# Kernel optimization log

Hardware: AMD Instinct MI355X
Metric: run time of the kernel (lower is better)

## Reference

```python
import jax, jax.numpy as jnp
import numpy as np

EPS = 1e-6
N_HEAD = 16

def alibi_slopes(n_head):
    # standard ALiBi geometric slopes for power-of-2 head counts
    start = 2.0 ** (-8.0 / n_head)
    return (start ** np.arange(1, n_head + 1)).astype(np.float32)

def rsig(x):
    # rational sigmoid sigma(x) = 0.5 * (x / (|x| + 1) + 1)
    return 0.5 * (x / (jnp.abs(x) + 1.0) + 1.0)

def mr_norm(x, w):
    # RationalMR: x / (mean(|x|) + eps) * weight
    return x / (jnp.mean(jnp.abs(x), axis=-1, keepdims=True) + EPS) * w


def setup_inputs() -> dict:
    key = jax.random.key(0)
    ks = jax.random.split(key, 6)
    d_model, d_ffn = 1024, 4096
    B, T = 1, 2048
    x = jax.random.normal(ks[0], (B, T, d_model), dtype=jnp.float32)
    s = 0.02
    w_qkv = jax.random.normal(ks[1], (3 * d_model, d_model), dtype=jnp.float32) * s
    w_out = jax.random.normal(ks[2], (d_model, d_model), dtype=jnp.float32) * s
    w_merged = jax.random.normal(ks[3], (2 * d_ffn, d_model), dtype=jnp.float32) * s
    w3 = jax.random.normal(ks[4], (d_model, d_ffn), dtype=jnp.float32) * s
    norm1_w = jnp.ones((d_model,), dtype=jnp.float32)
    norm2_w = jnp.ones((d_model,), dtype=jnp.float32)
    return {"x": x, "w_qkv": w_qkv, "w_out": w_out, "w_merged": w_merged,
            "w3": w3, "norm1_w": norm1_w, "norm2_w": norm2_w}


def reference(x, w_qkv, w_out, w_merged, w3, norm1_w, norm2_w):
    B, T, C = x.shape
    H = N_HEAD
    D = C // H
    scale = 1.0 / jnp.sqrt(jnp.float32(D))

    # --- attention sub-block ---
    h = mr_norm(x, norm1_w)
    qkv = (h @ w_qkv.T).reshape(B, T, 3, H, D).transpose(2, 0, 3, 1, 4)  # [3,B,H,T,D]
    q, k, v = qkv[0], qkv[1], qkv[2]
    scores = jnp.einsum('bhtd,bhsd->bhts', q, k) * scale  # [B,H,T,T]
    pos = jnp.arange(T)
    rel = jnp.abs(pos[:, None] - pos[None, :]).astype(jnp.float32)
    slopes = jnp.asarray(alibi_slopes(H))
    scores = scores - rel[None, None] * slopes[None, :, None, None]
    causal = pos[None, :] > pos[:, None]  # mask j > i
    scores = jnp.where(causal[None, None], jnp.float32(-10000.0), scores)
    # rational softmax: sigma(s)^4 / (sum sigma(s)^4 + eps)
    p4 = rsig(scores) ** 4
    probs = p4 / (jnp.sum(p4, axis=-1, keepdims=True) + EPS)
    attn = jnp.einsum('bhts,bhsd->bhtd', probs, v)  # [B,H,T,D]
    attn = attn.transpose(0, 2, 1, 3).reshape(B, T, C)
    x = x + attn @ w_out.T

    # --- FFN sub-block (rational SwiGLU) ---
    h2 = mr_norm(x, norm2_w)
    merged = h2 @ w_merged.T
    gate, val = jnp.split(merged, 2, axis=-1)
    hidden = gate * rsig(gate) * val
    x = x + hidden @ w3.T
    return x
```

## Files before the change

kernel.cpp:

```cpp
#include <hip/hip_runtime.h>
#include <hip/hip_bf16.h>
#include <stdint.h>

typedef unsigned int u32;
typedef unsigned short u16;
typedef __attribute__((ext_vector_type(8))) short bf16x8;
typedef __attribute__((ext_vector_type(4))) float f32x4;

#define MFMA(a, b, c) __builtin_amdgcn_mfma_f32_16x16x32_bf16(a, b, c, 0, 0, 0)

__device__ __forceinline__ u16 f2bf(float f) {
  u32 u = __float_as_uint(f);
  return (u16)((u + 0x7FFFu + ((u >> 16) & 1u)) >> 16);
}
__device__ __forceinline__ float bf2f(u16 h) {
  return __uint_as_float(((u32)h) << 16);
}
__device__ __forceinline__ float rsig_fast(float sc) {
  return 0.5f + 0.5f * sc * __builtin_amdgcn_rcpf(fabsf(sc) + 1.f);
}
__device__ __forceinline__ void async16(void* lds, const void* g) {
  __builtin_amdgcn_global_load_lds((const __attribute__((address_space(1))) u32*)g,
                                   (__attribute__((address_space(3))) u32*)lds, 16, 0, 0);
}

__global__ __launch_bounds__(256) void to_bf16_all(const float* __restrict__ s0, u16* __restrict__ d0,
                                                   const float* __restrict__ s1, u16* __restrict__ d1,
                                                   const float* __restrict__ s2, u16* __restrict__ d2,
                                                   const float* __restrict__ s3, u16* __restrict__ d3) {
  int b = blockIdx.x;
  const float* src; u16* dst;
  if (b < 1536)      { src = s0; dst = d0; }
  else if (b < 2048) { src = s1; dst = d1; b -= 1536; }
  else if (b < 6144) { src = s2; dst = d2; b -= 2048; }
  else               { src = s3; dst = d3; b -= 6144; }
  const size_t i = (size_t)b * 256 + threadIdx.x;
  const float4 a = ((const float4*)src)[2 * i];
  const float4 c = ((const float4*)src)[2 * i + 1];
  ushort4 o0, o1;
  o0.x = f2bf(a.x); o0.y = f2bf(a.y); o0.z = f2bf(a.z); o0.w = f2bf(a.w);
  o1.x = f2bf(c.x); o1.y = f2bf(c.y); o1.z = f2bf(c.z); o1.w = f2bf(c.w);
  ((ushort4*)dst)[2 * i] = o0;
  ((ushort4*)dst)[2 * i + 1] = o1;
}

__global__ __launch_bounds__(256) void mrnorm(const float* __restrict__ x,
                                              const float* __restrict__ wg,
                                              u16* __restrict__ out) {
  const int row = blockIdx.x;
  const int tid = threadIdx.x;
  const float4 v = ((const float4*)(x + (size_t)row * 1024))[tid];
  float s = fabsf(v.x) + fabsf(v.y) + fabsf(v.z) + fabsf(v.w);
#pragma unroll
  for (int off = 1; off < 64; off <<= 1) s += __shfl_xor(s, off);
  __shared__ float red[4];
  if ((tid & 63) == 0) red[tid >> 6] = s;
  __syncthreads();
  const float inv = 1.f / ((red[0] + red[1] + red[2] + red[3]) * (1.f / 1024.f) + 1e-6f);
  const float4 g = ((const float4*)wg)[tid];
  ushort4 o;
  o.x = f2bf(v.x * inv * g.x);
  o.y = f2bf(v.y * inv * g.y);
  o.z = f2bf(v.z * inv * g.z);
  o.w = f2bf(v.w * inv * g.w);
  ((ushort4*)out)[(size_t)row * 256 + tid] = o;
}

template <int EPI, bool DBUF>
__global__ __launch_bounds__(256) void gemm_bt(const u16* __restrict__ A, int lda,
                                               const u16* __restrict__ B, int ldb,
                                               void* __restrict__ C,
                                               const float* __restrict__ resid,
                                               int M, int N, int K) {
  __shared__ __align__(16) u16 As[(DBUF ? 2 : 1) * 128 * 64];
  __shared__ __align__(16) u16 Bs[(DBUF ? 2 : 1) * 128 * 64];
  const int tid = threadIdx.x;
  const int lane = tid & 63;
  const int w = tid >> 6;
  const int wr = (w >> 1) << 6;
  const int wc = (w & 1) << 6;
  const int nbn = N >> 7;
  const int m0 = (blockIdx.x / nbn) << 7;
  const int n0 = (blockIdx.x % nbn) << 7;
  const int l15 = lane & 15;
  const int lhi = lane >> 4;
  A += (size_t)blockIdx.y * K;
  B += (size_t)blockIdx.y * K;

  f32x4 acc[4][4] = {};

  auto stage = [&](int buf, int k0) {
#pragma unroll
    for (int p = 0; p < 4; ++p) {
      const int c = p * 256 + tid;
      const int row = c >> 3;
      const int cb = (c & 7) << 4;
      const int src = cb ^ ((row & 7) << 4);
      async16((char*)As + buf * 16384 + c * 16,
              (const char*)A + ((size_t)(m0 + row) * lda + k0) * 2 + src);
      async16((char*)Bs + buf * 16384 + c * 16,
              (const char*)B + ((size_t)(n0 + row) * ldb + k0) * 2 + src);
    }
  };
  auto compute = [&](int buf) {
#pragma unroll
    for (int kk = 0; kk < 2; ++kk) {
      bf16x8 af[4], bfr[4];
#pragma unroll
      for (int m = 0; m < 4; ++m) {
        const int row = wr + (m << 4) + l15;
        const int off = row * 128 + (((kk << 6) + (lhi << 4)) ^ ((row & 7) << 4));
        af[m] = *(const bf16x8*)((const char*)As + buf * 16384 + off);
      }
#pragma unroll
      for (int n = 0; n < 4; ++n) {
        const int row = wc + (n << 4) + l15;
        const int off = row * 128 + (((kk << 6) + (lhi << 4)) ^ ((row & 7) << 4));
        bfr[n] = *(const bf16x8*)((const char*)Bs + buf * 16384 + off);
      }
#pragma unroll
      for (int m = 0; m < 4; ++m)
#pragma unroll
        for (int n = 0; n < 4; ++n)
          acc[m][n] = MFMA(af[m], bfr[n], acc[m][n]);
    }
  };

  if (DBUF) {
    stage(0, 0);
    __syncthreads();
    int cur = 0;
    for (int k0 = 0; k0 < K; k0 += 64) {
      if (k0 + 64 < K) stage(cur ^ 1, k0 + 64);
      compute(cur);
      __syncthreads();
      cur ^= 1;
    }
  } else {
    for (int k0 = 0; k0 < K; k0 += 64) {
      stage(0, k0);
      __syncthreads();
      compute(0);
      __syncthreads();
    }
  }

  u16* Cp = (u16*)C + (size_t)blockIdx.y * M * N;
#pragma unroll
  for (int m = 0; m < 4; ++m) {
#pragma unroll
    for (int n = 0; n < 4; ++n) {
      const int col = n0 + wc + (n << 4) + l15;
#pragma unroll
      for (int r = 0; r < 4; ++r) {
        const int row = m0 + wr + (m << 4) + (lhi << 2) + r;
        const float v = acc[m][n][r];
        if (EPI == 0) {
          Cp[(size_t)row * N + col] = f2bf(v);
        } else {
          const size_t idx = (size_t)row * N + col;
          ((float*)C)[idx] = resid[idx] + v;
        }
      }
    }
  }
}

__global__ __launch_bounds__(256) void gemm_ffn1(const u16* __restrict__ A,
                                                 const u16* __restrict__ B,
                                                 u16* __restrict__ hid) {
  __shared__ __align__(16) u16 As[2][128 * 64];
  __shared__ __align__(16) u16 Bg[2][64 * 64];
  __shared__ __align__(16) u16 Bv[2][64 * 64];
  const int tid = threadIdx.x;
  const int lane = tid & 63;
  const int w = tid >> 6;
  const int wr = (w >> 1) << 6;
  const int wc = (w & 1) << 5;
  const int m0 = (blockIdx.x >> 6) << 7;
  const int n0 = (blockIdx.x & 63) << 6;
  const int l15 = lane & 15;
  const int lhi = lane >> 4;

  f32x4 ag[4][2] = {};
  f32x4 av[4][2] = {};

  auto stage = [&](int buf, int k0) {
#pragma unroll
    for (int p = 0; p < 4; ++p) {
      const int c = p * 256 + tid;
      const int row = c >> 3;
      const int cb = (c & 7) << 4;
      const int src = cb ^ ((row & 7) << 4);
      async16((char*)As[buf] + c * 16,
              (const char*)A + ((size_t)(m0 + row) * 1024 + k0) * 2 + src);
    }
#pragma unroll
    for (int p = 0; p < 2; ++p) {
      const int c = p * 256 + tid;
      const int row = c >> 3;
      const int cb = (c & 7) << 4;
      const int src = cb ^ ((row & 7) << 4);
      async16((char*)Bg[buf] + c * 16,
              (const char*)B + ((size_t)(n0 + row) * 1024 + k0) * 2 + src);
      async16((char*)Bv[buf] + c * 16,
              (const char*)B + ((size_t)(4096 + n0 + row) * 1024 + k0) * 2 + src);
    }
  };
  auto compute = [&](int buf) {
#pragma unroll
    for (int kk = 0; kk < 2; ++kk) {
      bf16x8 af[4], bgf[2], bvf[2];
#pragma unroll
      for (int m = 0; m < 4; ++m) {
        const int row = wr + (m << 4) + l15;
        const int off = row * 128 + (((kk << 6) + (lhi << 4)) ^ ((row & 7) << 4));
        af[m] = *(const bf16x8*)((const char*)As[buf] + off);
      }
#pragma unroll
      for (int n = 0; n < 2; ++n) {
        const int row = wc + (n << 4) + l15;
        const int off = row * 128 + (((kk << 6) + (lhi << 4)) ^ ((row & 7) << 4));
        bgf[n] = *(const bf16x8*)((const char*)Bg[buf] + off);
        bvf[n] = *(const bf16x8*)((const char*)Bv[buf] + off);
      }
#pragma unroll
      for (int m = 0; m < 4; ++m)
#pragma unroll
        for (int n = 0; n < 2; ++n) {
          ag[m][n] = MFMA(af[m], bgf[n], ag[m][n]);
          av[m][n] = MFMA(af[m], bvf[n], av[m][n]);
        }
    }
  };

  stage(0, 0);
  __syncthreads();
  int cur = 0;
  for (int k0 = 0; k0 < 1024; k0 += 64) {
    if (k0 + 64 < 1024) stage(cur ^ 1, k0 + 64);
    compute(cur);
    __syncthreads();
    cur ^= 1;
  }

#pragma unroll
  for (int m = 0; m < 4; ++m) {
#pragma unroll
    for (int n = 0; n < 2; ++n) {
      const int col = n0 + wc + (n << 4) + l15;
#pragma unroll
      for (int r = 0; r < 4; ++r) {
        const int row = m0 + wr + (m << 4) + (lhi << 2) + r;
        const float g = ag[m][n][r];
        const float v = av[m][n][r];
        hid[(size_t)row * 4096 + col] = f2bf(g * rsig_fast(g) * v);
      }
    }
  }
}

template <int NC, bool BF16OUT>
__global__ __launch_bounds__(256) void splitk_reduce(const u16* __restrict__ part,
                                                     size_t cstride,
                                                     const float* __restrict__ resid,
                                                     void* __restrict__ out) {
  const size_t i = ((size_t)blockIdx.x * 256 + threadIdx.x) * 8;
  float acc[8];
  if constexpr (BF16OUT) {
#pragma unroll
    for (int j = 0; j < 8; ++j) acc[j] = 0.f;
  } else {
    const float4 r0 = *(const float4*)(resid + i);
    const float4 r1 = *(const float4*)(resid + i + 4);
    acc[0] = r0.x; acc[1] = r0.y; acc[2] = r0.z; acc[3] = r0.w;
    acc[4] = r1.x; acc[5] = r1.y; acc[6] = r1.z; acc[7] = r1.w;
  }
#pragma unroll
  for (int c = 0; c < NC; ++c) {
    const uint4 p = *(const uint4*)(part + (size_t)c * cstride + i);
    const u16* ps = (const u16*)&p;
#pragma unroll
    for (int j = 0; j < 8; ++j) acc[j] += bf2f(ps[j]);
  }
  if constexpr (BF16OUT) {
    u16 ob[8];
#pragma unroll
    for (int j = 0; j < 8; ++j) ob[j] = f2bf(acc[j]);
    *(uint4*)((u16*)out + i) = *(const uint4*)ob;
  } else {
    float4 o0 = {acc[0], acc[1], acc[2], acc[3]};
    float4 o1 = {acc[4], acc[5], acc[6], acc[7]};
    *(float4*)((float*)out + i) = o0;
    *(float4*)((float*)out + i + 4) = o1;
  }
}

__global__ __launch_bounds__(256) void transpose_v(const u16* __restrict__ qkv,
                                                   u16* __restrict__ vt) {
  __shared__ __align__(16) u16 tile[64][72];
  const int head = blockIdx.x >> 5;
  const int t0 = (blockIdx.x & 31) << 6;
  const int tid = threadIdx.x;
  const int row = tid >> 2;
  const int cb = (tid & 3) << 4;
  const u16* src = qkv + (size_t)(t0 + row) * 3072 + 2048 + head * 64 + cb;
  *(uint4*)&tile[row][cb] = *(const uint4*)src;
  *(uint4*)&tile[row][cb + 8] = *(const uint4*)(src + 8);
  __syncthreads();
  u16 buf[16];
#pragma unroll
  for (int j = 0; j < 16; ++j) buf[j] = tile[cb + j][row];
  u16* dst = vt + (size_t)(head * 64 + row) * 2048 + t0 + cb;
  *(uint4*)dst = *(const uint4*)&buf[0];
  *(uint4*)(dst + 8) = *(const uint4*)&buf[8];
}

__global__ __launch_bounds__(256) void attn_part(const u16* __restrict__ qkv,
                                                 const u16* __restrict__ vt,
                                                 u16* __restrict__ pnum,
                                                 float* __restrict__ pden) {
  const int id = blockIdx.x;
  const int head = id & 15;
  const int rem = id >> 4;
  int a, g;
  if (rem < 32)      { a = 3; g = rem; }
  else if (rem < 56) { a = 2; g = rem - 32; }
  else if (rem < 72) { a = 1; g = rem - 56; }
  else               { a = 0; g = rem - 72; }
  const int qb = (a << 3) + g / (a + 1);
  const int c = g - (g / (a + 1)) * (a + 1);
  const int slot = head * 80 + ((a * (a + 1)) << 2) + (qb - (a << 3)) * (a + 1) + c;

  __shared__ __align__(16) u16 Ks[2][64 * 64];
  __shared__ __align__(16) u16 Vs[2][64 * 64];
  __shared__ __align__(16) u16 QP[4][16 * 64];
  const int tid = threadIdx.x;
  const int lane = tid & 63;
  const int w = tid >> 6;
  const int l15 = lane & 15;
  const int lhi = lane >> 4;
  const int qbase = qb << 6;
  const float slope = exp2f(-0.5f * (float)(head + 1));

  auto stageKV = [&](int buf, int s0) {
#pragma unroll
    for (int p = 0; p < 2; ++p) {
      const int cc = p * 256 + tid;
      const int row = cc >> 3;
      const int cb = (cc & 7) << 4;
      const int src = cb ^ ((row & 7) << 4);
      async16((char*)Ks[buf] + cc * 16,
              (const char*)qkv + ((size_t)(s0 + row) * 3072 + 1024 + head * 64) * 2 + src);
      async16((char*)Vs[buf] + cc * 16,
              (const char*)vt + ((size_t)(head * 64 + row) * 2048 + s0) * 2 + src);
    }
  };

  const int sfirst = c << 9;
  const int smax = min(qbase, sfirst + 448);
#pragma unroll
  for (int p = 0; p < 2; ++p) {
    const int cc = p * 256 + tid;
    const int row = cc >> 3;
    const int cb = (cc & 7) << 4;
    const int src = cb ^ ((row & 7) << 4);
    async16((char*)QP + cc * 16,
            (const char*)qkv + ((size_t)(qbase + row) * 3072 + head * 64) * 2 + src);
  }
  stageKV(0, sfirst);
  __syncthreads();

  bf16x8 qf[2];
#pragma unroll
  for (int kk = 0; kk < 2; ++kk) {
    const int row = (w << 4) + l15;
    const int off = row * 128 + (((kk << 6) + (lhi << 4)) ^ ((row & 7) << 4));
    qf[kk] = *(const bf16x8*)((const char*)QP + off);
  }

  f32x4 oacc[4] = {};
  float rs[4] = {0.f, 0.f, 0.f, 0.f};
  u16* pw = (u16*)QP[w];
  int cur = 0;

  for (int s0 = sfirst; s0 <= smax; s0 += 64) {
    if (s0 + 64 <= smax) stageKV(cur ^ 1, s0 + 64);
    const char* Kc = (const char*)Ks[cur];
    const char* Vc = (const char*)Vs[cur];

    bf16x8 kf[4][2];
#pragma unroll
    for (int bb = 0; bb < 4; ++bb)
#pragma unroll
      for (int kk = 0; kk < 2; ++kk) {
        const int row = (bb << 4) + l15;
        const int off = row * 128 + (((kk << 6) + (lhi << 4)) ^ ((row & 7) << 4));
        kf[bb][kk] = *(const bf16x8*)(Kc + off);
      }
    f32x4 sa[4];
#pragma unroll
    for (int bb = 0; bb < 4; ++bb) {
      f32x4 z = {0.f, 0.f, 0.f, 0.f};
      z = MFMA(qf[0], kf[bb][0], z);
      sa[bb] = MFMA(qf[1], kf[bb][1], z);
    }
#pragma unroll
    for (int bb = 0; bb < 4; ++bb) {
      const int s_abs = s0 + (bb << 4) + l15;
#pragma unroll
      for (int r = 0; r < 4; ++r) {
        const int prow = (lhi << 2) + r;
        const int q_abs = qbase + (w << 4) + prow;
        float p4 = 0.f;
        if (s_abs <= q_abs) {
          const float sc = sa[bb][r] * 0.125f - slope * (float)(q_abs - s_abs);
          const float t = rsig_fast(sc);
          const float t2 = t * t;
          p4 = t2 * t2;
        }
        rs[r] += p4;
        const int pcol2 = ((bb << 4) + l15) << 1;
        const int poff = prow * 128 + (pcol2 ^ ((prow & 7) << 4));
        *(u16*)((char*)pw + poff) = f2bf(p4);
      }
    }
    bf16x8 pf[2];
#pragma unroll
    for (int kk = 0; kk < 2; ++kk) {
      const int row = l15;
      const int off = row * 128 + (((kk << 6) + (lhi << 4)) ^ ((row & 7) << 4));
      pf[kk] = *(const bf16x8*)((const char*)pw + off);
    }
#pragma unroll
    for (int db = 0; db < 4; ++db) {
#pragma unroll
      for (int kk = 0; kk < 2; ++kk) {
        const int row = (db << 4) + l15;
        const int off = row * 128 + (((kk << 6) + (lhi << 4)) ^ ((row & 7) << 4));
        const bf16x8 vf = *(const bf16x8*)(Vc + off);
        oacc[db] = MFMA(pf[kk], vf, oacc[db]);
      }
    }
    __syncthreads();
    cur ^= 1;
  }

#pragma unroll
  for (int r = 0; r < 4; ++r) {
    float v = rs[r];
    v += __shfl_xor(v, 1);
    v += __shfl_xor(v, 2);
    v += __shfl_xor(v, 4);
    v += __shfl_xor(v, 8);
    rs[r] = v;
  }
  if (l15 == 0) {
#pragma unroll
    for (int r = 0; r < 4; ++r)
      pden[(size_t)slot * 64 + (w << 4) + (lhi << 2) + r] = rs[r];
  }
  __syncthreads();
#pragma unroll
  for (int db = 0; db < 4; ++db)
#pragma unroll
    for (int r = 0; r < 4; ++r)
      pw[((lhi << 2) + r) * 64 + (db << 4) + l15] = f2bf(oacc[db][r]);
  __syncthreads();
  {
    const int row = lane >> 2;
    const int cb = (lane & 3) << 4;
    const u16* s = pw + row * 64 + cb;
    const uint4 d0 = *(const uint4*)s;
    const uint4 d1 = *(const uint4*)(s + 8);
    u16* dst = pnum + (size_t)slot * 4096 + ((w << 4) + row) * 64 + cb;
    *(uint4*)dst = d0;
    *(uint4*)(dst + 8) = d1;
  }
}

__global__ __launch_bounds__(256) void attn_merge(const u16* __restrict__ pnum,
                                                  const float* __restrict__ pden,
                                                  u16* __restrict__ out) {
  const int head = blockIdx.x >> 5;
  const int qb = blockIdx.x & 31;
  const int nc = (qb >> 3) + 1;
  const int a = qb >> 3, b = qb & 7;
  const int slot0 = head * 80 + ((a * (a + 1)) << 2) + b * (a + 1);
  const int tid = threadIdx.x;
  const int row = tid >> 2;
  const int c0 = (tid & 3) << 4;

  float acc[16] = {};
  float den = 0.f;
  for (int ci = 0; ci < nc; ++ci) {
    const int slot = slot0 + ci;
    den += pden[(size_t)slot * 64 + row];
    const u16* np = pnum + (size_t)slot * 4096 + row * 64 + c0;
    const uint4 n0 = *(const uint4*)np;
    const uint4 n1 = *(const uint4*)(np + 8);
    const u16* ns0 = (const u16*)&n0;
    const u16* ns1 = (const u16*)&n1;
#pragma unroll
    for (int j = 0; j < 8; ++j) {
      acc[j] += bf2f(ns0[j]);
      acc[8 + j] += bf2f(ns1[j]);
    }
  }
  const float inv = 1.f / (den + 1e-6f);
  u16 ob[16];
#pragma unroll
  for (int j = 0; j < 16; ++j) ob[j] = f2bf(acc[j] * inv);
  u16* dst = out + (size_t)((qb << 6) + row) * 1024 + head * 64 + c0;
  *(uint4*)dst = *(const uint4*)&ob[0];
  *(uint4*)(dst + 8) = *(const uint4*)&ob[8];
}

extern "C" void kernel_launch(void* const* d_in, const int* in_sizes, int n_in,
                              void* d_out, int out_size, void* d_ws, size_t ws_size,
                              hipStream_t stream) {
  const float* x     = (const float*)d_in[0];
  const float* wqkv  = (const float*)d_in[1];
  const float* wout  = (const float*)d_in[2];
  const float* wmer  = (const float*)d_in[3];
  const float* w3    = (const float*)d_in[4];
  const float* n1w   = (const float*)d_in[5];
  const float* n2w   = (const float*)d_in[6];
  char* ws = (char*)d_ws;

  u16*   WQKV = (u16*)(ws + 0);
  u16*   WOUT = (u16*)(ws + 6291456);
  u16*   WMER = (u16*)(ws + 8388608);
  u16*   W3B  = (u16*)(ws + 25165824);
  u16*   H    = (u16*)(ws + 33554432);
  u16*   QKV  = (u16*)(ws + 37748736);
  u16*   VT   = (u16*)(ws + 50331648);
  u16*   PNUM = (u16*)(ws + 54525952);
  float* PDEN = (float*)(ws + 65011712);
  u16*   ATTN = (u16*)(ws + 65536000);
  u16*   WOP  = (u16*)(ws + 37748736);
  float* X1   = (float*)(ws + 54525952);
  u16*   H2   = (u16*)(ws + 33554432);
  u16*   HID  = (u16*)(ws + 37748736);
  u16*   W3P  = (u16*)(ws + 62914560);

  to_bf16_all<<<8192, 256, 0, stream>>>(wqkv, WQKV, wout, WOUT, wmer, WMER, w3, W3B);

  mrnorm<<<2048, 256, 0, stream>>>(x, n1w, H);
  gemm_bt<0, true><<<16 * 24, 256, 0, stream>>>(H, 1024, WQKV, 1024, QKV, nullptr,
                                                2048, 3072, 1024);
  transpose_v<<<512, 256, 0, stream>>>(QKV, VT);
  attn_part<<<1280, 256, 0, stream>>>(QKV, VT, PNUM, PDEN);
  attn_merge<<<512, 256, 0, stream>>>(PNUM, PDEN, ATTN);
  gemm_bt<0, true><<<dim3(16 * 8, 4), 256, 0, stream>>>(ATTN, 1024, WOUT, 1024, WOP,
                                                        nullptr, 2048, 1024, 256);
  splitk_reduce<4, false><<<1024, 256, 0, stream>>>(WOP, 2097152, x, X1);

  mrnorm<<<2048, 256, 0, stream>>>(X1, n2w, H2);
  gemm_ffn1<<<1024, 256, 0, stream>>>(H2, WMER, HID);
  gemm_bt<0, true><<<dim3(16 * 8, 4), 256, 0, stream>>>(HID, 4096, W3B, 4096, W3P,
                                                        nullptr, 2048, 1024, 1024);
  splitk_reduce<4, false><<<1024, 256, 0, stream>>>(W3P, 2097152, X1, (float*)d_out);
}
```

Baseline: 172.5 us.

## Enlarge attention query tile to 128 rows with 512-thread blocks

```diff
diff --git a/kernel.cpp b/kernel.cpp
--- a/kernel.cpp
+++ b/kernel.cpp
@@ -316,52 +316,47 @@
   *(uint4*)(dst + 8) = *(const uint4*)&buf[8];
 }
 
-__global__ __launch_bounds__(256) void attn_part(const u16* __restrict__ qkv,
+__global__ __launch_bounds__(512) void attn_part(const u16* __restrict__ qkv,
                                                  const u16* __restrict__ vt,
                                                  u16* __restrict__ pnum,
                                                  float* __restrict__ pden) {
   const int id = blockIdx.x;
   const int head = id & 15;
   const int rem = id >> 4;
-  int a, g;
-  if (rem < 32)      { a = 3; g = rem; }
-  else if (rem < 56) { a = 2; g = rem - 32; }
-  else if (rem < 72) { a = 1; g = rem - 56; }
-  else               { a = 0; g = rem - 72; }
-  const int qb = (a << 3) + g / (a + 1);
-  const int c = g - (g / (a + 1)) * (a + 1);
-  const int slot = head * 80 + ((a * (a + 1)) << 2) + (qb - (a << 3)) * (a + 1) + c;
+  int qb2, c;
+  if (rem < 4)       { qb2 = 4 + rem;                          c = 0; }
+  else if (rem < 12) { const int t = rem - 4;  qb2 = 8 + (t >> 1);  c = t & 1; }
+  else if (rem < 24) { const int t = rem - 12; qb2 = 12 + t / 3;    c = t % 3; }
+  else               { const int t = rem - 24; qb2 = ((t & 3) << 2) + 3 - (t >> 2); c = qb2 >> 2; }
+  const int a2 = qb2 >> 2, b2 = qb2 & 3;
+  const int slot = head * 40 + ((a2 * (a2 + 1)) << 1) + b2 * (a2 + 1) + c;
 
   __shared__ __align__(16) u16 Ks[2][64 * 64];
   __shared__ __align__(16) u16 Vs[2][64 * 64];
-  __shared__ __align__(16) u16 QP[4][16 * 64];
+  __shared__ __align__(16) u16 QP[8][16 * 64];
   const int tid = threadIdx.x;
   const int lane = tid & 63;
   const int w = tid >> 6;
   const int l15 = lane & 15;
   const int lhi = lane >> 4;
-  const int qbase = qb << 6;
+  const int qbase = qb2 << 7;
   const float slope = exp2f(-0.5f * (float)(head + 1));
 
   auto stageKV = [&](int buf, int s0) {
-#pragma unroll
-    for (int p = 0; p < 2; ++p) {
-      const int cc = p * 256 + tid;
-      const int row = cc >> 3;
-      const int cb = (cc & 7) << 4;
-      const int src = cb ^ ((row & 7) << 4);
-      async16((char*)Ks[buf] + cc * 16,
-              (const char*)qkv + ((size_t)(s0 + row) * 3072 + 1024 + head * 64) * 2 + src);
-      async16((char*)Vs[buf] + cc * 16,
-              (const char*)vt + ((size_t)(head * 64 + row) * 2048 + s0) * 2 + src);
-    }
+    const int row = tid >> 3;
+    const int cb = (tid & 7) << 4;
+    const int src = cb ^ ((row & 7) << 4);
+    async16((char*)Ks[buf] + tid * 16,
+            (const char*)qkv + ((size_t)(s0 + row) * 3072 + 1024 + head * 64) * 2 + src);
+    async16((char*)Vs[buf] + tid * 16,
+            (const char*)vt + ((size_t)(head * 64 + row) * 2048 + s0) * 2 + src);
   };
 
   const int sfirst = c << 9;
-  const int smax = min(qbase, sfirst + 448);
+  const int smax = min(qbase + 64, sfirst + 448);
 #pragma unroll
   for (int p = 0; p < 2; ++p) {
-    const int cc = p * 256 + tid;
+    const int cc = p * 512 + tid;
     const int row = cc >> 3;
     const int cb = (cc & 7) << 4;
     const int src = cb ^ ((row & 7) << 4);
@@ -458,7 +453,7 @@
   if (l15 == 0) {
 #pragma unroll
     for (int r = 0; r < 4; ++r)
-      pden[(size_t)slot * 64 + (w << 4) + (lhi << 2) + r] = rs[r];
+      pden[(size_t)slot * 128 + (w << 4) + (lhi << 2) + r] = rs[r];
   }
   __syncthreads();
 #pragma unroll
@@ -473,7 +468,7 @@
     const u16* s = pw + row * 64 + cb;
     const uint4 d0 = *(const uint4*)s;
     const uint4 d1 = *(const uint4*)(s + 8);
-    u16* dst = pnum + (size_t)slot * 4096 + ((w << 4) + row) * 64 + cb;
+    u16* dst = pnum + (size_t)slot * 8192 + ((w << 4) + row) * 64 + cb;
     *(uint4*)dst = d0;
     *(uint4*)(dst + 8) = d1;
   }
@@ -484,19 +479,21 @@
                                                   u16* __restrict__ out) {
   const int head = blockIdx.x >> 5;
   const int qb = blockIdx.x & 31;
-  const int nc = (qb >> 3) + 1;
-  const int a = qb >> 3, b = qb & 7;
-  const int slot0 = head * 80 + ((a * (a + 1)) << 2) + b * (a + 1);
+  const int qb2 = qb >> 1;
+  const int a2 = qb >> 3;
+  const int nc = a2 + 1;
+  const int slot0 = head * 40 + ((a2 * (a2 + 1)) << 1) + (qb2 & 3) * (a2 + 1);
   const int tid = threadIdx.x;
   const int row = tid >> 2;
   const int c0 = (tid & 3) << 4;
+  const int rr = ((qb & 1) << 6) + row;
 
   float acc[16] = {};
   float den = 0.f;
   for (int ci = 0; ci < nc; ++ci) {
     const int slot = slot0 + ci;
-    den += pden[(size_t)slot * 64 + row];
-    const u16* np = pnum + (size_t)slot * 4096 + row * 64 + c0;
+    den += pden[(size_t)slot * 128 + rr];
+    const u16* np = pnum + (size_t)slot * 8192 + rr * 64 + c0;
     const uint4 n0 = *(const uint4*)np;
     const uint4 n1 = *(const uint4*)(np + 8);
     const u16* ns0 = (const u16*)&n0;
@@ -550,7 +547,7 @@
   gemm_bt<0, true><<<16 * 24, 256, 0, stream>>>(H, 1024, WQKV, 1024, QKV, nullptr,
                                                 2048, 3072, 1024);
   transpose_v<<<512, 256, 0, stream>>>(QKV, VT);
-  attn_part<<<1280, 256, 0, stream>>>(QKV, VT, PNUM, PDEN);
+  attn_part<<<640, 512, 0, stream>>>(QKV, VT, PNUM, PDEN);
   attn_merge<<<512, 256, 0, stream>>>(PNUM, PDEN, ATTN);
   gemm_bt<0, true><<<dim3(16 * 8, 4), 256, 0, stream>>>(ATTN, 1024, WOUT, 1024, WOP,
                                                         nullptr, 2048, 1024, 256);
```

Result: faster. 165.8 us (-3.8%).
